# Kernel optimization log

Measured on AMD Instinct MI355X. Metric: run time of the kernel, lower is better.

## Reference

```python
import jax, jax.numpy as jnp
import numpy as np

B, OBS, H, N = 16384, 512, 1024, 9

def setup_inputs() -> dict:
    key = jax.random.key(0)
    ks = jax.random.split(key, 12)
    s = 0.02
    return {
        "obs": jax.random.normal(ks[0], (B, OBS), jnp.float32),
        "agent_positions": jax.random.normal(ks[1], (B, N, 3), jnp.float32),
        "W1": jax.random.normal(ks[2], (OBS, H), jnp.float32) * s,
        "b1": jnp.zeros((H,), jnp.float32),
        "W2": jax.random.normal(ks[3], (H, H), jnp.float32) * s,
        "b2": jnp.zeros((H,), jnp.float32),
        "Wc1": jax.random.normal(ks[4], (H, H // 2), jnp.float32) * s,
        "bc1": jnp.zeros((H // 2,), jnp.float32),
        "Wc2": jax.random.normal(ks[5], (H // 2, 1), jnp.float32) * s,
        "bc2": jnp.zeros((1,), jnp.float32),
        "Wt1": jax.random.normal(ks[6], (H, H // 2), jnp.float32) * s,
        "bt1": jnp.zeros((H // 2,), jnp.float32),
        "Wt2": jax.random.normal(ks[7], (H // 2, 1), jnp.float32) * s,
        "bt2": jnp.zeros((1,), jnp.float32),
        "Wk1": jax.random.normal(ks[8], (2 * H, H), jnp.float32) * s,
        "bk1": jnp.zeros((H,), jnp.float32),
        "Wk2": jax.random.normal(ks[9], (H, 1), jnp.float32) * s,
        "bk2": jnp.zeros((1,), jnp.float32),
    }


def reference(obs, agent_positions, W1, b1, W2, b2, Wc1, bc1, Wc2, bc2,
              Wt1, bt1, Wt2, bt2, Wk1, bk1, Wk2, bk2):
    # global features: Linear->ReLU->Linear->ReLU
    g = jax.nn.relu(obs @ W1 + b1)
    g = jax.nn.relu(g @ W2 + b2)  # [B, H]

    # Each per-agent head is applied to the SAME g in the original loop,
    # so one pass + broadcast is mathematically identical.
    cov = jax.nn.sigmoid(jax.nn.relu(g @ Wc1 + bc1) @ Wc2 + bc2)  # [B,1]
    trk = jax.nn.sigmoid(jax.nn.relu(g @ Wt1 + bt1) @ Wt2 + bt2)  # [B,1]
    coop_in = jnp.concatenate([g, g], axis=-1)                    # [B,2H]
    coop = jax.nn.sigmoid(jax.nn.relu(coop_in @ Wk1 + bk1) @ Wk2 + bk2)  # [B,1]
    # mean over 8 identical cooperation scores == the score itself

    coverage = jnp.broadcast_to(cov, (cov.shape[0], N))      # [B, N]
    tracking = jnp.broadcast_to(trk, (trk.shape[0], N))      # [B, N]
    cooperation = jnp.broadcast_to(coop, (coop.shape[0], N)) # [B, N]
    return (coverage, tracking, cooperation)
```

## Files before the change

kernel.cpp:

```cpp
#include <hip/hip_runtime.h>
#include <hip/hip_bf16.h>

#define B_ROWS 16384
#define OBS_D  512
#define H_D    1024
#define N_AG   9

typedef __attribute__((ext_vector_type(8))) short short8;
typedef __attribute__((ext_vector_type(4))) float floatx4;

__device__ __forceinline__ unsigned short f_to_bf_raw(float f) {
  union { float f; unsigned u; } c; c.f = f;
  unsigned u = c.u;
  u = u + 0x7FFF + ((u >> 16) & 1);
  return (unsigned short)(u >> 16);
}

__device__ __forceinline__ size_t frag_off(int n, int k, int KT) {
  const int ft = (n >> 4) * KT + (k >> 5);
  const int ln = (n & 15) | (((k >> 3) & 3) << 4);
  return ((size_t)ft * 64 + ln) * 8 + (k & 7);
}

__global__ __launch_bounds__(256) void prep_all(
    const float* __restrict__ obs,
    const float* __restrict__ W1, const float* __restrict__ W2,
    const float* __restrict__ Wc1, const float* __restrict__ Wt1,
    const float* __restrict__ Wk1,
    const float* __restrict__ bc1, const float* __restrict__ bt1,
    const float* __restrict__ bk1,
    const float* __restrict__ Wc2, const float* __restrict__ Wt2,
    const float* __restrict__ Wk2,
    unsigned short* __restrict__ obs_bf,
    unsigned short* __restrict__ W1f, unsigned short* __restrict__ W2f,
    unsigned short* __restrict__ WHf,
    float* __restrict__ bias2048, float* __restrict__ w2cat) {
  __shared__ float t[32][33];
  const int bx  = blockIdx.x;
  const int tid = threadIdx.x;

  if (bx < 4096) {
    int i = (bx * 256 + tid) * 8;
    float4 a = *(const float4*)(obs + i);
    float4 b = *(const float4*)(obs + i + 4);
    short8 o;
    o[0] = (short)f_to_bf_raw(a.x); o[1] = (short)f_to_bf_raw(a.y);
    o[2] = (short)f_to_bf_raw(a.z); o[3] = (short)f_to_bf_raw(a.w);
    o[4] = (short)f_to_bf_raw(b.x); o[5] = (short)f_to_bf_raw(b.y);
    o[6] = (short)f_to_bf_raw(b.z); o[7] = (short)f_to_bf_raw(b.w);
    *(short8*)(obs_bf + i) = o;
    return;
  }

  const int tx = tid & 31;
  const int ty = tid >> 5;

  if (bx < 4608) {
    const int tt = bx - 4096;
    const int k0 = (tt & 15) * 32;
    const int n0 = (tt >> 4) * 32;
#pragma unroll
    for (int i = ty; i < 32; i += 8)
      t[i][tx] = W1[(size_t)(k0 + i) * 1024 + n0 + tx];
    __syncthreads();
#pragma unroll
    for (int i = ty; i < 32; i += 8)
      W1f[frag_off(n0 + i, k0 + tx, 16)] = f_to_bf_raw(t[tx][i]);
    return;
  }

  if (bx < 5632) {
    const int tt = bx - 4608;
    const int k0 = (tt & 31) * 32;
    const int n0 = (tt >> 5) * 32;
#pragma unroll
    for (int i = ty; i < 32; i += 8)
      t[i][tx] = W2[(size_t)(k0 + i) * 1024 + n0 + tx];
    __syncthreads();
#pragma unroll
    for (int i = ty; i < 32; i += 8)
      W2f[frag_off(n0 + i, k0 + tx, 32)] = f_to_bf_raw(t[tx][i]);
    return;
  }

  if (bx < 7680) {
    const int tt = bx - 5632;
    const int k0 = (tt & 31) * 32;
    const int n0 = (tt >> 5) * 32;
#pragma unroll
    for (int i = ty; i < 32; i += 8) {
      const int n = n0 + tx;
      float v;
      if (n0 < 512)
        v = Wc1[(size_t)(k0 + i) * 512 + n];
      else if (n0 < 1024)
        v = Wt1[(size_t)(k0 + i) * 512 + (n - 512)];
      else
        v = Wk1[(size_t)(k0 + i) * 1024 + (n - 1024)]
          + Wk1[(size_t)(k0 + i + 1024) * 1024 + (n - 1024)];
      t[i][tx] = v;
    }
    __syncthreads();
#pragma unroll
    for (int i = ty; i < 32; i += 8)
      WHf[frag_off(n0 + i, k0 + tx, 32)] = f_to_bf_raw(t[tx][i]);
    return;
  }

  {
    int n = (bx - 7680) * 256 + tid;
    float b, w;
    if (n < 512)       { b = bc1[n];        w = Wc2[n]; }
    else if (n < 1024) { b = bt1[n - 512];  w = Wt2[n - 512]; }
    else               { b = bk1[n - 1024]; w = Wk2[n - 1024]; }
    bias2048[n] = b;
    w2cat[n] = w;
  }
}

#define GLD_LDS(gp, lp)                                                        \
  __builtin_amdgcn_global_load_lds(                                            \
      (const __attribute__((address_space(1))) void*)(gp),                     \
      (__attribute__((address_space(3))) void*)(lp), 16, 0, 0)

#define GEMM_CORE_V7(ACC_DECL)                                                 \
  __shared__ __align__(16) unsigned short As[2][128 * 32];          \
  const int tid  = threadIdx.x;                                                \
  const int lane = tid & 63;                                                   \
  const int wave = tid >> 6;                                                   \
  const int m0 = blockIdx.x * 128;                                             \
  const int n0 = blockIdx.y * 128;                                             \
  const int wm = (wave & 1) * 64;                                              \
  const int wn = (wave >> 1) * 64;                                             \
  const int fr = lane & 15;                                                    \
  const int fq = lane >> 4;                                                    \
  ACC_DECL;                                                                    \
  constexpr int KT = K >> 5;                                                   \
  constexpr int nIter = KT;                                                    \
  const size_t rowb = (size_t)K * 2;                                           \
  const int srow   = lane >> 2;                                                \
  const int schunk = (lane & 3) ^ ((srow >> 1) & 3);                           \
  const char* gA0 = (const char*)A + (size_t)(m0 + wave * 32 + srow) * rowb    \
                    + schunk * 16;                                             \
  const char* gA1 = gA0 + 16 * rowb;                                           \
  char* lA = (char*)&As[0][0] + (wave * 32) * 64 + lane * 16;                  \
  const char* gBf = (const char*)Bf                                            \
      + (((size_t)((n0 >> 4) + (wn >> 4)) * KT) * 64 + lane) * 16;             \
  const int fswz = (fr >> 1) & 3;                                              \
  const int fsA = (wm + fr) * 64 + ((fq ^ fswz) * 16);                         \
  short8 Fa[2][4], Fb[2][4];                                                   \
      \
  GLD_LDS(gA0, lA); GLD_LDS(gA1, lA + 1024);                                   \
  gA0 += 64; gA1 += 64;                                                        \
  __syncthreads();                                                             \
  GLD_LDS(gA0, lA + 8192); GLD_LDS(gA1, lA + 9216);                            \
  gA0 += 64; gA1 += 64;                                                        \
  _Pragma("unroll")                                                            \
  for (int ni = 0; ni < 4; ++ni)                                               \
    Fb[0][ni] = *(const short8*)(gBf + (size_t)ni * (KT * 1024));              \
  _Pragma("unroll")                                                            \
  for (int mi = 0; mi < 4; ++mi)                                               \
    Fa[0][mi] = *(const short8*)((const char*)&As[0][0] + fsA + mi * 1024);    \
  _Pragma("unroll")                                                            \
  for (int k = 0; k < nIter; ++k) {        \
    const int cur = k & 1;                     \
    __syncthreads();                                                           \
    if (k + 2 < nIter) {                                                       \
      char* dA = lA + cur * 8192;                                              \
      GLD_LDS(gA0, dA); GLD_LDS(gA1, dA + 1024);                               \
      gA0 += 64; gA1 += 64;                                                    \
    }                                                                          \
    if (k + 1 < nIter) {                                                       \
      _Pragma("unroll")                                                        \
      for (int ni = 0; ni < 4; ++ni)                                           \
        Fb[cur ^ 1][ni] =                                                      \
            *(const short8*)(gBf + ((size_t)ni * KT + (k + 1)) * 1024);        \
      const char* bAs = (const char*)&As[0][0] + (cur ^ 1) * 8192;             \
      _Pragma("unroll")                                                        \
      for (int mi = 0; mi < 4; ++mi)                                           \
        Fa[cur ^ 1][mi] = *(const short8*)(bAs + fsA + mi * 1024);             \
    }                                                                          \
    _Pragma("unroll")                                                          \
    for (int mi = 0; mi < 4; ++mi)                                             \
      _Pragma("unroll")                                                        \
      for (int ni = 0; ni < 4; ++ni)                                           \
        acc[mi][ni] = __builtin_amdgcn_mfma_f32_16x16x32_bf16(                 \
            Fa[cur][mi], Fb[cur][ni], acc[mi][ni], 0, 0, 0);                   \
  }

#define ACC_INIT                                                               \
  floatx4 acc[4][4];                                                           \
  _Pragma("unroll")                                                            \
  for (int i = 0; i < 4; ++i)                                                  \
    _Pragma("unroll")                                                          \
    for (int j = 0; j < 4; ++j) acc[i][j] = (floatx4){0.f, 0.f, 0.f, 0.f}

template <int K>
__global__ __launch_bounds__(256, 3) void gemm_bias_relu(
    const unsigned short* __restrict__ A,
    const unsigned short* __restrict__ Bf,
    const float* __restrict__ bias,
    unsigned short* __restrict__ C,
    int M, int N) {
  GEMM_CORE_V7(ACC_INIT)

#pragma unroll
  for (int ni = 0; ni < 4; ++ni) {
    const int gn = n0 + wn + ni * 16 + fr;
    const float bv = bias[gn];
#pragma unroll
    for (int mi = 0; mi < 4; ++mi) {
#pragma unroll
      for (int r = 0; r < 4; ++r) {
        const int gm = m0 + wm + mi * 16 + fq * 4 + r;
        float v = acc[mi][ni][r] + bv;
        v = v > 0.f ? v : 0.f;
        C[(size_t)gm * N + gn] = f_to_bf_raw(v);
      }
    }
  }
}

template <int K>
__global__ __launch_bounds__(256, 3) void gemm_heads_fused(
    const unsigned short* __restrict__ A,
    const unsigned short* __restrict__ Bf,
    const float* __restrict__ bias,
    const float* __restrict__ w2,
    float* __restrict__ part,
    int M, int N) {
  GEMM_CORE_V7(ACC_INIT)

  const int j = blockIdx.y * 2 + (wave >> 1);
  float w2v[4], bv[4];
#pragma unroll
  for (int ni = 0; ni < 4; ++ni) {
    const int gn = n0 + wn + ni * 16 + fr;
    w2v[ni] = w2[gn];
    bv[ni]  = bias[gn];
  }
#pragma unroll
  for (int mi = 0; mi < 4; ++mi) {
#pragma unroll
    for (int r = 0; r < 4; ++r) {
      float p = 0.f;
#pragma unroll
      for (int ni = 0; ni < 4; ++ni) {
        float v = acc[mi][ni][r] + bv[ni];
        v = v > 0.f ? v : 0.f;
        p += v * w2v[ni];
      }
      p += __shfl_xor(p, 1);
      p += __shfl_xor(p, 2);
      p += __shfl_xor(p, 4);
      p += __shfl_xor(p, 8);
      if (fr == 0) {
        const int gm = m0 + wm + mi * 16 + fq * 4 + r;
        part[(size_t)j * B_ROWS + gm] = p;
      }
    }
  }
}

__global__ __launch_bounds__(256) void final_out(
    const float* __restrict__ part,
    const float* __restrict__ bc2, const float* __restrict__ bt2,
    const float* __restrict__ bk2, float* __restrict__ out) {
  const int row = blockIdx.x * 256 + threadIdx.x;
  float sc = 0.f, st = 0.f, sk = 0.f;
#pragma unroll
  for (int j = 0; j < 8; ++j)  sc += part[(size_t)j * B_ROWS + row];
#pragma unroll
  for (int j = 8; j < 16; ++j) st += part[(size_t)j * B_ROWS + row];
#pragma unroll
  for (int j = 16; j < 32; ++j) sk += part[(size_t)j * B_ROWS + row];
  const float cv = 1.f / (1.f + expf(-(sc + bc2[0])));
  const float tv = 1.f / (1.f + expf(-(st + bt2[0])));
  const float kv = 1.f / (1.f + expf(-(sk + bk2[0])));
  float* o0 = out + (size_t)row * N_AG;
  float* o1 = out + (size_t)(B_ROWS + row) * N_AG;
  float* o2 = out + (size_t)(2 * B_ROWS + row) * N_AG;
#pragma unroll
  for (int a = 0; a < N_AG; ++a) { o0[a] = cv; o1[a] = tv; o2[a] = kv; }
}

extern "C" void kernel_launch(void* const* d_in, const int* in_sizes, int n_in,
                              void* d_out, int out_size, void* d_ws, size_t ws_size,
                              hipStream_t stream) {
  const float* obs = (const float*)d_in[0];
  const float* W1  = (const float*)d_in[2];
  const float* b1  = (const float*)d_in[3];
  const float* W2  = (const float*)d_in[4];
  const float* b2  = (const float*)d_in[5];
  const float* Wc1 = (const float*)d_in[6];
  const float* bc1 = (const float*)d_in[7];
  const float* Wc2 = (const float*)d_in[8];
  const float* bc2 = (const float*)d_in[9];
  const float* Wt1 = (const float*)d_in[10];
  const float* bt1 = (const float*)d_in[11];
  const float* Wt2 = (const float*)d_in[12];
  const float* bt2 = (const float*)d_in[13];
  const float* Wk1 = (const float*)d_in[14];
  const float* bk1 = (const float*)d_in[15];
  const float* Wk2 = (const float*)d_in[16];
  const float* bk2 = (const float*)d_in[17];
  float* out = (float*)d_out;

  char* ws = (char*)d_ws;
  unsigned short* obs_bf  = (unsigned short*)(ws + 0);
  float*          PART    = (float*)(ws + 0);
  unsigned short* W1f     = (unsigned short*)(ws + 16777216);
  unsigned short* W2f     = (unsigned short*)(ws + 17825792);
  unsigned short* WHf     = (unsigned short*)(ws + 19922944);
  float*          bias2048= (float*)(ws + 24117248);
  float*          w2cat   = (float*)(ws + 24125440);
  unsigned short* G1      = (unsigned short*)(ws + 24330240);
  unsigned short* G       = (unsigned short*)(ws + 57884672);

  prep_all<<<7688, 256, 0, stream>>>(obs, W1, W2, Wc1, Wt1, Wk1,
                                     bc1, bt1, bk1, Wc2, Wt2, Wk2,
                                     obs_bf, W1f, W2f, WHf, bias2048, w2cat);

  gemm_bias_relu<512><<<dim3(128, 8), 256, 0, stream>>>(obs_bf, W1f, b1, G1, B_ROWS, 1024);
  gemm_bias_relu<1024><<<dim3(128, 8), 256, 0, stream>>>(G1, W2f, b2, G, B_ROWS, 1024);

  gemm_heads_fused<1024><<<dim3(128, 16), 256, 0, stream>>>(G, WHf, bias2048, w2cat, PART,
                                                            B_ROWS, 2048);

  final_out<<<B_ROWS / 256, 256, 0, stream>>>(PART, bc2, bt2, bk2, out);
}
```

Measured before the change: 278.5 us.

## Store activations in MFMA fragment layout and load A directly to registers

```diff
diff --git a/kernel.cpp b/kernel.cpp
--- a/kernel.cpp
+++ b/kernel.cpp
@@ -16,9 +16,9 @@
   return (unsigned short)(u >> 16);
 }
 
-__device__ __forceinline__ size_t frag_off(int n, int k, int KT) {
-  const int ft = (n >> 4) * KT + (k >> 5);
-  const int ln = (n & 15) | (((k >> 3) & 3) << 4);
+__device__ __forceinline__ size_t frag_off(int r, int k, int KT) {
+  const int ft = (r >> 4) * KT + (k >> 5);
+  const int ln = (r & 15) | (((k >> 3) & 3) << 4);
   return ((size_t)ft * 64 + ln) * 8 + (k & 7);
 }
 
@@ -31,7 +31,7 @@
     const float* __restrict__ bk1,
     const float* __restrict__ Wc2, const float* __restrict__ Wt2,
     const float* __restrict__ Wk2,
-    unsigned short* __restrict__ obs_bf,
+    unsigned short* __restrict__ obs_f,
     unsigned short* __restrict__ W1f, unsigned short* __restrict__ W2f,
     unsigned short* __restrict__ WHf,
     float* __restrict__ bias2048, float* __restrict__ w2cat) {
@@ -40,15 +40,21 @@
   const int tid = threadIdx.x;
 
   if (bx < 4096) {
-    int i = (bx * 256 + tid) * 8;
-    float4 a = *(const float4*)(obs + i);
-    float4 b = *(const float4*)(obs + i + 4);
+    const int id   = bx * 256 + tid;
+    const int lane = id & 63;
+    const int ft   = id >> 6;
+    const int mt   = ft >> 4;
+    const int kt   = ft & 15;
+    const int m    = mt * 16 + (lane & 15);
+    const int k0   = kt * 32 + (lane >> 4) * 8;
+    float4 a = *(const float4*)(obs + (size_t)m * 512 + k0);
+    float4 b = *(const float4*)(obs + (size_t)m * 512 + k0 + 4);
     short8 o;
     o[0] = (short)f_to_bf_raw(a.x); o[1] = (short)f_to_bf_raw(a.y);
     o[2] = (short)f_to_bf_raw(a.z); o[3] = (short)f_to_bf_raw(a.w);
     o[4] = (short)f_to_bf_raw(b.x); o[5] = (short)f_to_bf_raw(b.y);
     o[6] = (short)f_to_bf_raw(b.z); o[7] = (short)f_to_bf_raw(b.w);
-    *(short8*)(obs_bf + i) = o;
+    *(short8*)(obs_f + ((size_t)ft * 64 + lane) * 8) = o;
     return;
   }
 
@@ -118,67 +124,48 @@
   }
 }
 
-#define GLD_LDS(gp, lp)                                                        \
-  __builtin_amdgcn_global_load_lds(                                            \
-      (const __attribute__((address_space(1))) void*)(gp),                     \
-      (__attribute__((address_space(3))) void*)(lp), 16, 0, 0)
-
-#define GEMM_CORE_V7(ACC_DECL)                                                 \
-  __shared__ __align__(16) unsigned short As[2][128 * 32];          \
+#define GEMM_CORE_V8(ACC_DECL)                                                 \
   const int tid  = threadIdx.x;                                                \
   const int lane = tid & 63;                                                   \
   const int wave = tid >> 6;                                                   \
-  const int m0 = blockIdx.x * 128;                                             \
-  const int n0 = blockIdx.y * 128;                                             \
+  constexpr int nper = NT / 8;                                                 \
+  const int xcd  = blockIdx.x & 7;                                             \
+  const int rest = blockIdx.x >> 3;                                            \
+  const int n_t  = xcd * nper + (rest % nper);                                 \
+  const int m_t  = rest / nper;                                                \
+  const int m0 = m_t * 128;                                                    \
+  const int n0 = n_t * 128;                                                    \
   const int wm = (wave & 1) * 64;                                              \
   const int wn = (wave >> 1) * 64;                                             \
   const int fr = lane & 15;                                                    \
   const int fq = lane >> 4;                                                    \
   ACC_DECL;                                                                    \
   constexpr int KT = K >> 5;                                                   \
-  constexpr int nIter = KT;                                                    \
-  const size_t rowb = (size_t)K * 2;                                           \
-  const int srow   = lane >> 2;                                                \
-  const int schunk = (lane & 3) ^ ((srow >> 1) & 3);                           \
-  const char* gA0 = (const char*)A + (size_t)(m0 + wave * 32 + srow) * rowb    \
-                    + schunk * 16;                                             \
-  const char* gA1 = gA0 + 16 * rowb;                                           \
-  char* lA = (char*)&As[0][0] + (wave * 32) * 64 + lane * 16;                  \
-  const char* gBf = (const char*)Bf                                            \
-      + (((size_t)((n0 >> 4) + (wn >> 4)) * KT) * 64 + lane) * 16;             \
-  const int fswz = (fr >> 1) & 3;                                              \
-  const int fsA = (wm + fr) * 64 + ((fq ^ fswz) * 16);                         \
-  short8 Fa[2][4], Fb[2][4];                                                   \
-      \
-  GLD_LDS(gA0, lA); GLD_LDS(gA1, lA + 1024);                                   \
-  gA0 += 64; gA1 += 64;                                                        \
-  __syncthreads();                                                             \
-  GLD_LDS(gA0, lA + 8192); GLD_LDS(gA1, lA + 9216);                            \
-  gA0 += 64; gA1 += 64;                                                        \
+  const unsigned short* gA =                                                   \
+      Af + ((size_t)(((m0 + wm) >> 4) * KT) * 64 + lane) * 8;                  \
+  const unsigned short* gB =                                                   \
+      Bf + ((size_t)(((n0 + wn) >> 4) * KT) * 64 + lane) * 8;                  \
+  short8 Fa[3][4], Fb[3][4];                                                   \
   _Pragma("unroll")                                                            \
-  for (int ni = 0; ni < 4; ++ni)                                               \
-    Fb[0][ni] = *(const short8*)(gBf + (size_t)ni * (KT * 1024));              \
+  for (int p = 0; p < 2; ++p) {                                                \
+    _Pragma("unroll")                                                          \
+    for (int mi = 0; mi < 4; ++mi)                                             \
+      Fa[p][mi] = *(const short8*)(gA + ((size_t)mi * KT + p) * 512);          \
+    _Pragma("unroll")                                                          \
+    for (int ni = 0; ni < 4; ++ni)                                             \
+      Fb[p][ni] = *(const short8*)(gB + ((size_t)ni * KT + p) * 512);          \
+  }                                                                            \
   _Pragma("unroll")                                                            \
-  for (int mi = 0; mi < 4; ++mi)                                               \
-    Fa[0][mi] = *(const short8*)((const char*)&As[0][0] + fsA + mi * 1024);    \
-  _Pragma("unroll")                                                            \
-  for (int k = 0; k < nIter; ++k) {        \
-    const int cur = k & 1;                     \
-    __syncthreads();                                                           \
-    if (k + 2 < nIter) {                                                       \
-      char* dA = lA + cur * 8192;                                              \
-      GLD_LDS(gA0, dA); GLD_LDS(gA1, dA + 1024);                               \
-      gA0 += 64; gA1 += 64;                                                    \
-    }                                                                          \
-    if (k + 1 < nIter) {                                                       \
+  for (int k = 0; k < KT; ++k) {           \
+    const int cur = k % 3;                                                     \
+    if (k + 2 < KT) {                                                          \
+      const int nxt = (k + 2) % 3;                                             \
+      _Pragma("unroll")                                                        \
+      for (int mi = 0; mi < 4; ++mi)                                           \
+        Fa[nxt][mi] = *(const short8*)(gA + ((size_t)mi * KT + k + 2) * 512);  \
       _Pragma("unroll")                                                        \
       for (int ni = 0; ni < 4; ++ni)                                           \
-        Fb[cur ^ 1][ni] =                                                      \
-            *(const short8*)(gBf + ((size_t)ni * KT + (k + 1)) * 1024);        \
-      const char* bAs = (const char*)&As[0][0] + (cur ^ 1) * 8192;             \
-      _Pragma("unroll")                                                        \
-      for (int mi = 0; mi < 4; ++mi)                                           \
-        Fa[cur ^ 1][mi] = *(const short8*)(bAs + fsA + mi * 1024);             \
+        Fb[nxt][ni] = *(const short8*)(gB + ((size_t)ni * KT + k + 2) * 512);  \
     }                                                                          \
     _Pragma("unroll")                                                          \
     for (int mi = 0; mi < 4; ++mi)                                             \
@@ -195,43 +182,63 @@
     _Pragma("unroll")                                                          \
     for (int j = 0; j < 4; ++j) acc[i][j] = (floatx4){0.f, 0.f, 0.f, 0.f}
 
-template <int K>
-__global__ __launch_bounds__(256, 3) void gemm_bias_relu(
-    const unsigned short* __restrict__ A,
+template <int K, int NT>
+__global__ __launch_bounds__(256, 2) void gemm_bias_relu(
+    const unsigned short* __restrict__ Af,
     const unsigned short* __restrict__ Bf,
     const float* __restrict__ bias,
-    unsigned short* __restrict__ C,
-    int M, int N) {
-  GEMM_CORE_V7(ACC_INIT)
-
-#pragma unroll
-  for (int ni = 0; ni < 4; ++ni) {
-    const int gn = n0 + wn + ni * 16 + fr;
-    const float bv = bias[gn];
-#pragma unroll
-    for (int mi = 0; mi < 4; ++mi) {
-#pragma unroll
-      for (int r = 0; r < 4; ++r) {
-        const int gm = m0 + wm + mi * 16 + fq * 4 + r;
-        float v = acc[mi][ni][r] + bv;
-        v = v > 0.f ? v : 0.f;
-        C[(size_t)gm * N + gn] = f_to_bf_raw(v);
+    unsigned short* __restrict__ Cf) {
+  GEMM_CORE_V8(ACC_INIT)
+
+  constexpr int KT2 = (NT * 128) / 32;
+  __shared__ unsigned short eps[64][136];
+  float bv[4];
+#pragma unroll
+  for (int ni = 0; ni < 4; ++ni) bv[ni] = bias[n0 + wn + ni * 16 + fr];
+
+#pragma unroll
+  for (int p = 0; p < 2; ++p) {
+    if (p) __syncthreads();
+#pragma unroll
+    for (int h = 0; h < 2; ++h) {
+      const int mi = 2 * p + h;
+#pragma unroll
+      for (int ni = 0; ni < 4; ++ni) {
+#pragma unroll
+        for (int r = 0; r < 4; ++r) {
+          float v = acc[mi][ni][r] + bv[ni];
+          v = v > 0.f ? v : 0.f;
+          eps[(wm >> 1) + h * 16 + fq * 4 + r][wn + ni * 16 + fr] =
+              f_to_bf_raw(v);
+        }
       }
     }
-  }
-}
-
-template <int K>
-__global__ __launch_bounds__(256, 3) void gemm_heads_fused(
-    const unsigned short* __restrict__ A,
+    __syncthreads();
+#pragma unroll
+    for (int s = 0; s < 4; ++s) {
+      const int slot = s * 4 + wave;
+      const int tl   = slot >> 2;
+      const int ktl  = slot & 3;
+      const int Lrow = tl * 16 + (lane & 15);
+      const int ncol = ktl * 32 + (lane >> 4) * 8;
+      short8 v = *(const short8*)&eps[Lrow][ncol];
+      const int gmt = (m0 >> 4) + ((tl >> 1) * 4) + 2 * p + (tl & 1);
+      const int gkt = (n0 >> 5) + ktl;
+      *(short8*)(Cf + ((size_t)(gmt * KT2 + gkt) * 64 + lane) * 8) = v;
+    }
+  }
+}
+
+template <int K, int NT>
+__global__ __launch_bounds__(256, 2) void gemm_heads_fused(
+    const unsigned short* __restrict__ Af,
     const unsigned short* __restrict__ Bf,
     const float* __restrict__ bias,
     const float* __restrict__ w2,
-    float* __restrict__ part,
-    int M, int N) {
-  GEMM_CORE_V7(ACC_INIT)
-
-  const int j = blockIdx.y * 2 + (wave >> 1);
+    float* __restrict__ part) {
+  GEMM_CORE_V8(ACC_INIT)
+
+  const int j = n_t * 2 + (wave >> 1);
   float w2v[4], bv[4];
 #pragma unroll
   for (int ni = 0; ni < 4; ++ni) {
@@ -307,7 +314,7 @@
   float* out = (float*)d_out;
 
   char* ws = (char*)d_ws;
-  unsigned short* obs_bf  = (unsigned short*)(ws + 0);
+  unsigned short* obs_f   = (unsigned short*)(ws + 0);
   float*          PART    = (float*)(ws + 0);
   unsigned short* W1f     = (unsigned short*)(ws + 16777216);
   unsigned short* W2f     = (unsigned short*)(ws + 17825792);
@@ -319,13 +326,12 @@
 
   prep_all<<<7688, 256, 0, stream>>>(obs, W1, W2, Wc1, Wt1, Wk1,
                                      bc1, bt1, bk1, Wc2, Wt2, Wk2,
-                                     obs_bf, W1f, W2f, WHf, bias2048, w2cat);
-
-  gemm_bias_relu<512><<<dim3(128, 8), 256, 0, stream>>>(obs_bf, W1f, b1, G1, B_ROWS, 1024);
-  gemm_bias_relu<1024><<<dim3(128, 8), 256, 0, stream>>>(G1, W2f, b2, G, B_ROWS, 1024);
-
-  gemm_heads_fused<1024><<<dim3(128, 16), 256, 0, stream>>>(G, WHf, bias2048, w2cat, PART,
-                                                            B_ROWS, 2048);
+                                     obs_f, W1f, W2f, WHf, bias2048, w2cat);
+
+  gemm_bias_relu<512, 8><<<1024, 256, 0, stream>>>(obs_f, W1f, b1, G1);
+  gemm_bias_relu<1024, 8><<<1024, 256, 0, stream>>>(G1, W2f, b2, G);
+
+  gemm_heads_fused<1024, 16><<<2048, 256, 0, stream>>>(G, WHf, bias2048, w2cat, PART);
 
   final_out<<<B_ROWS / 256, 256, 0, stream>>>(PART, bc2, bt2, bk2, out);
 }
```

Result: slower. 361.3 us (+29.7%).

## Deepen GEMM K-step to 64 with triple-buffered LDS A tiles

Applied to the files above, without the earlier changes.

```diff
diff --git a/kernel.cpp b/kernel.cpp
--- a/kernel.cpp
+++ b/kernel.cpp
@@ -16,8 +16,8 @@
   return (unsigned short)(u >> 16);
 }
 
-__device__ __forceinline__ size_t frag_off(int n, int k, int KT) {
-  const int ft = (n >> 4) * KT + (k >> 5);
+__device__ __forceinline__ size_t frag_off(int n, int k, int KT32) {
+  const int ft = (n >> 4) * KT32 + (k >> 5);
   const int ln = (n & 15) | (((k >> 3) & 3) << 4);
   return ((size_t)ft * 64 + ln) * 8 + (k & 7);
 }
@@ -123,8 +123,8 @@
       (const __attribute__((address_space(1))) void*)(gp),                     \
       (__attribute__((address_space(3))) void*)(lp), 16, 0, 0)
 
-#define GEMM_CORE_V7(ACC_DECL)                                                 \
-  __shared__ __align__(16) unsigned short As[2][128 * 32];          \
+#define GEMM_CORE_V9(ACC_DECL)                                                 \
+  __shared__ __align__(16) unsigned short As[3][128 * 64];          \
   const int tid  = threadIdx.x;                                                \
   const int lane = tid & 63;                                                   \
   const int wave = tid >> 6;                                                   \
@@ -135,57 +135,71 @@
   const int fr = lane & 15;                                                    \
   const int fq = lane >> 4;                                                    \
   ACC_DECL;                                                                    \
-  constexpr int KT = K >> 5;                                                   \
-  constexpr int nIter = KT;                                                    \
+  constexpr int KT   = K >> 6;                      \
+  constexpr int KT32 = K >> 5;                      \
   const size_t rowb = (size_t)K * 2;                                           \
-  const int srow   = lane >> 2;                                                \
-  const int schunk = (lane & 3) ^ ((srow >> 1) & 3);                           \
-  const char* gA0 = (const char*)A + (size_t)(m0 + wave * 32 + srow) * rowb    \
-                    + schunk * 16;                                             \
-  const char* gA1 = gA0 + 16 * rowb;                                           \
-  char* lA = (char*)&As[0][0] + (wave * 32) * 64 + lane * 16;                  \
-  const char* gBf = (const char*)Bf                                            \
-      + (((size_t)((n0 >> 4) + (wn >> 4)) * KT) * 64 + lane) * 16;             \
-  const int fswz = (fr >> 1) & 3;                                              \
-  const int fsA = (wm + fr) * 64 + ((fq ^ fswz) * 16);                         \
-  short8 Fa[2][4], Fb[2][4];                                                   \
-      \
-  GLD_LDS(gA0, lA); GLD_LDS(gA1, lA + 1024);                                   \
-  gA0 += 64; gA1 += 64;                                                        \
-  __syncthreads();                                                             \
-  GLD_LDS(gA0, lA + 8192); GLD_LDS(gA1, lA + 9216);                            \
-  gA0 += 64; gA1 += 64;                                                        \
-  _Pragma("unroll")                                                            \
-  for (int ni = 0; ni < 4; ++ni)                                               \
-    Fb[0][ni] = *(const short8*)(gBf + (size_t)ni * (KT * 1024));              \
-  _Pragma("unroll")                                                            \
-  for (int mi = 0; mi < 4; ++mi)                                               \
-    Fa[0][mi] = *(const short8*)((const char*)&As[0][0] + fsA + mi * 1024);    \
-  _Pragma("unroll")                                                            \
-  for (int k = 0; k < nIter; ++k) {        \
-    const int cur = k & 1;                     \
-    __syncthreads();                                                           \
-    if (k + 2 < nIter) {                                                       \
-      char* dA = lA + cur * 8192;                                              \
-      GLD_LDS(gA0, dA); GLD_LDS(gA1, dA + 1024);                               \
-      gA0 += 64; gA1 += 64;                                                    \
+  const int srow8  = lane >> 3;                   \
+  const int schunk = (lane & 7) ^ srow8;          \
+  const char* gA = (const char*)A + (size_t)(m0 + wave * 32 + srow8) * rowb    \
+                   + schunk * 16;                                              \
+  char* lA = (char*)&As[0][0] + wave * 4096 + lane * 16;                       \
+  const unsigned short* gB =                                                   \
+      Bf + ((size_t)(((n0 + wn) >> 4) * KT32) * 64 + lane) * 8;                \
+  const int fsA = (wm + fr) * 128;                                             \
+  const int sl0 = ((fq)     ^ (fr & 7)) * 16;                                  \
+  const int sl1 = ((4 + fq) ^ (fr & 7)) * 16;                                  \
+  short8 FbP[2][2][4];                                                         \
+                  \
+  _Pragma("unroll")                                                            \
+  for (int j = 0; j < 4; ++j)                                                  \
+    GLD_LDS(gA + (size_t)j * 8 * rowb, lA + j * 1024);                         \
+  _Pragma("unroll")                                                            \
+  for (int j = 0; j < 4; ++j)                                                  \
+    GLD_LDS(gA + 128 + (size_t)j * 8 * rowb,                                   \
+            (char*)&As[1][0] + wave * 4096 + lane * 16 + j * 1024);            \
+  _Pragma("unroll")                                                            \
+  for (int s = 0; s < 2; ++s)                                                  \
+    _Pragma("unroll")                                                          \
+    for (int ni = 0; ni < 4; ++ni)                                             \
+      FbP[0][s][ni] = *(const short8*)(gB + ((size_t)ni * KT32 + s) * 512);    \
+  _Pragma("unroll")                                                            \
+  for (int k = 0; k < KT; ++k) {           \
+    __syncthreads();            \
+    if (k + 2 < KT) {                                                          \
+      char* d = (char*)&As[(k + 2) % 3][0] + wave * 4096 + lane * 16;          \
+      const char* g = gA + (size_t)(k + 2) * 128;                              \
+      _Pragma("unroll")                                                        \
+      for (int j = 0; j < 4; ++j)                                              \
+        GLD_LDS(g + (size_t)j * 8 * rowb, d + j * 1024);                       \
     }                                                                          \
-    if (k + 1 < nIter) {                                                       \
+    if (k + 1 < KT) {                                                          \
       _Pragma("unroll")                                                        \
-      for (int ni = 0; ni < 4; ++ni)                                           \
-        Fb[cur ^ 1][ni] =                                                      \
-            *(const short8*)(gBf + ((size_t)ni * KT + (k + 1)) * 1024);        \
-      const char* bAs = (const char*)&As[0][0] + (cur ^ 1) * 8192;             \
-      _Pragma("unroll")                                                        \
-      for (int mi = 0; mi < 4; ++mi)                                           \
-        Fa[cur ^ 1][mi] = *(const short8*)(bAs + fsA + mi * 1024);             \
+      for (int s = 0; s < 2; ++s)                                              \
+        _Pragma("unroll")                                                      \
+        for (int ni = 0; ni < 4; ++ni)                                         \
+          FbP[(k + 1) & 1][s][ni] = *(const short8*)                           \
+              (gB + ((size_t)ni * KT32 + 2 * (k + 1) + s) * 512);              \
     }                                                                          \
+    const char* bA = (const char*)&As[k % 3][0];                               \
+    short8 Fa0[4], Fa1[4];                                                     \
+    _Pragma("unroll")                                                          \
+    for (int mi = 0; mi < 4; ++mi)                                             \
+      Fa0[mi] = *(const short8*)(bA + fsA + mi * 2048 + sl0);                  \
+    _Pragma("unroll")                                                          \
+    for (int mi = 0; mi < 4; ++mi)                                             \
+      Fa1[mi] = *(const short8*)(bA + fsA + mi * 2048 + sl1);                  \
     _Pragma("unroll")                                                          \
     for (int mi = 0; mi < 4; ++mi)                                             \
       _Pragma("unroll")                                                        \
       for (int ni = 0; ni < 4; ++ni)                                           \
         acc[mi][ni] = __builtin_amdgcn_mfma_f32_16x16x32_bf16(                 \
-            Fa[cur][mi], Fb[cur][ni], acc[mi][ni], 0, 0, 0);                   \
+            Fa0[mi], FbP[k & 1][0][ni], acc[mi][ni], 0, 0, 0);                 \
+    _Pragma("unroll")                                                          \
+    for (int mi = 0; mi < 4; ++mi)                                             \
+      _Pragma("unroll")                                                        \
+      for (int ni = 0; ni < 4; ++ni)                                           \
+        acc[mi][ni] = __builtin_amdgcn_mfma_f32_16x16x32_bf16(                 \
+            Fa1[mi], FbP[k & 1][1][ni], acc[mi][ni], 0, 0, 0);                 \
   }
 
 #define ACC_INIT                                                               \
@@ -196,13 +210,13 @@
     for (int j = 0; j < 4; ++j) acc[i][j] = (floatx4){0.f, 0.f, 0.f, 0.f}
 
 template <int K>
-__global__ __launch_bounds__(256, 3) void gemm_bias_relu(
+__global__ __launch_bounds__(256, 2) void gemm_bias_relu(
     const unsigned short* __restrict__ A,
     const unsigned short* __restrict__ Bf,
     const float* __restrict__ bias,
     unsigned short* __restrict__ C,
     int M, int N) {
-  GEMM_CORE_V7(ACC_INIT)
+  GEMM_CORE_V9(ACC_INIT)
 
 #pragma unroll
   for (int ni = 0; ni < 4; ++ni) {
@@ -222,14 +236,14 @@
 }
 
 template <int K>
-__global__ __launch_bounds__(256, 3) void gemm_heads_fused(
+__global__ __launch_bounds__(256, 2) void gemm_heads_fused(
     const unsigned short* __restrict__ A,
     const unsigned short* __restrict__ Bf,
     const float* __restrict__ bias,
     const float* __restrict__ w2,
     float* __restrict__ part,
     int M, int N) {
-  GEMM_CORE_V7(ACC_INIT)
+  GEMM_CORE_V9(ACC_INIT)
 
   const int j = blockIdx.y * 2 + (wave >> 1);
   float w2v[4], bv[4];
```

Result: faster. 251.2 us (-9.8%).
